# Optimization experiments

Measured on AMD Instinct MI355X. Metric: run time of the kernel, lower is better.

The kernel has to match this reference:

```python
import jax, jax.numpy as jnp
import numpy as np

D_IN, D_HID, D_OUT, N_EXP, N_TOK = 1024, 4096, 1024, 8, 4096


def setup_inputs() -> dict:
    key = jax.random.key(0)
    ks = jax.random.split(key, 7)
    x = jax.random.normal(ks[0], (N_TOK, D_IN), dtype=jnp.float32)
    s1 = 1.0 / np.sqrt(D_IN).astype(np.float32)
    s2 = 1.0 / np.sqrt(D_HID).astype(np.float32)
    W1 = jax.random.uniform(ks[1], (N_EXP, D_IN, D_HID), jnp.float32, -s1, s1)
    b1 = jax.random.uniform(ks[2], (N_EXP, D_HID), jnp.float32, -s1, s1)
    W2 = jax.random.uniform(ks[3], (N_EXP, D_HID, D_OUT), jnp.float32, -s2, s2)
    b2 = jax.random.uniform(ks[4], (N_EXP, D_OUT), jnp.float32, -s2, s2)
    Wg = jax.random.uniform(ks[5], (D_IN, N_EXP), jnp.float32, -s1, s1)
    bg = jax.random.uniform(ks[6], (N_EXP,), jnp.float32, -s1, s1)
    return {"x": x, "W1": W1, "b1": b1, "W2": W2, "b2": b2,
            "Wg": Wg, "bg": bg, "top_k": 2}


def reference(x, W1, b1, W2, b2, Wg, bg, top_k):
    # Gating: softmax over experts, then top-k and renormalizing softmax.
    gates = jax.nn.softmax(x @ Wg + bg, axis=-1)            # [N, E]
    topk_vals, topk_idx = jax.lax.top_k(gates, top_k)       # [N, k]
    topk_w = jax.nn.softmax(topk_vals, axis=-1)             # [N, k]
    # Dense all-expert MLP (vectorized replacement for per-token Python loop).
    h = jax.nn.relu(jnp.einsum('nd,edh->neh', x, W1) + b1)  # [N, E, H]
    y = jnp.einsum('neh,eho->neo', h, W2) + b2              # [N, E, O]
    # Combine: gather each token's top-k expert outputs, weighted sum.
    sel = jnp.take_along_axis(y, topk_idx[:, :, None], axis=1)  # [N, k, O]
    out = jnp.sum(topk_w[:, :, None] * sel, axis=1)             # [N, O]
    return out
```

## Files before the change

### kernel.cpp

```cpp
#include <hip/hip_runtime.h>
#include <hip/hip_bf16.h>

#define NTOK 4096
#define DIN  1024
#define DHID 4096
#define DOUT 1024
#define NEXP 8
#define TMAX 72
#define G1BLK (TMAX * (DHID / 128))
#define SPLITK 2
#define KH (DHID / SPLITK)

typedef __hip_bfloat16 bf16;
typedef short short8 __attribute__((ext_vector_type(8)));
typedef short short4v __attribute__((ext_vector_type(4)));
typedef float floatx4 __attribute__((ext_vector_type(4)));

#define WAIT_VM0 0x0F70
#define WAIT_VM4 0x0F74

#define WS_XB    0ull
#define WS_W1T   8388608ull
#define WS_W2T   75497472ull
#define WS_H     142606336ull
#define WS_META  209715200ull
#define MO_CNT    0
#define MO_CURG   32
#define MO_T2I    1536
#define MO_T2W    34304
#define MO_ROWS   67072
#define MO_ROWW   99840

__device__ __forceinline__ void gload16(const bf16* g, bf16* l) {
  __builtin_amdgcn_global_load_lds(
      (const __attribute__((address_space(1))) void*)g,
      (__attribute__((address_space(3))) void*)l, 16, 0, 0);
}

__device__ __forceinline__ int tile_lookup(const int* __restrict__ cnt, int tile,
                                           int& e, int& start, int& mrows) {
  int o = 0, tacc = 0;
  e = -1; start = 0; mrows = 0;
  #pragma unroll
  for (int k = 0; k < 8; k++) {
    int c = cnt[k];
    int nb = (c + 127) >> 7;
    if (e < 0 && tile < tacc + nb) {
      e = k; int r = (tile - tacc) << 7;
      start = o + r; mrows = min(128, c - r);
    }
    tacc += nb; o += c;
  }
  return tacc;
}

__device__ __forceinline__ void transpose_tile(const float* __restrict__ in,
                                               bf16* __restrict__ out,
                                               int R, int C, int cx, int ry,
                                               int e, float* t) {
  size_t ebase = (size_t)e * R * C;
  int c0 = cx * 64, r0 = ry * 64;
  int tid = threadIdx.x;
  int rr = tid >> 4;
  int cq = (tid & 15) * 4;
  #pragma unroll
  for (int i = 0; i < 4; i++) {
    int r = rr + i * 16;
    float4 v = *(const float4*)(in + ebase + (size_t)(r0 + r) * C + c0 + cq);
    t[(cq + 0) * 65 + r] = v.x; t[(cq + 1) * 65 + r] = v.y;
    t[(cq + 2) * 65 + r] = v.z; t[(cq + 3) * 65 + r] = v.w;
  }
  __syncthreads();
  int cc = tid >> 3;
  int rq = (tid & 7) * 8;
  #pragma unroll
  for (int i = 0; i < 2; i++) {
    int c = cc + i * 32;
    union { int4 v; bf16 h[8]; } u;
    #pragma unroll
    for (int j = 0; j < 8; j++) u.h[j] = __float2bfloat16(t[c * 65 + rq + j]);
    *(int4*)(out + ebase + (size_t)(c0 + c) * R + r0 + rq) = u.v;
  }
}

__device__ __forceinline__ void gate_body(const float* __restrict__ x,
                                          const float* __restrict__ Wg,
                                          const float* __restrict__ bg,
                                          bf16* __restrict__ xb,
                                          int* __restrict__ t2i,
                                          float* __restrict__ t2w,
                                          int* __restrict__ cnt, int blk) {
  int wave = threadIdx.x >> 6, lane = threadIdx.x & 63;
  int t = blk * 4 + wave;
  const float* xr = x + (size_t)t * DIN;
  bf16* xbr = xb + (size_t)t * DIN;
  float acc[8] = {0.f, 0.f, 0.f, 0.f, 0.f, 0.f, 0.f, 0.f};
  #pragma unroll
  for (int i = 0; i < 4; i++) {
    int d0 = (lane + i * 64) * 4;
    float4 v = *(const float4*)(xr + d0);
    union { short4v s; bf16 h[4]; } u;
    u.h[0] = __float2bfloat16(v.x); u.h[1] = __float2bfloat16(v.y);
    u.h[2] = __float2bfloat16(v.z); u.h[3] = __float2bfloat16(v.w);
    *(short4v*)(xbr + d0) = u.s;
    float xv4[4] = {v.x, v.y, v.z, v.w};
    #pragma unroll
    for (int c = 0; c < 4; c++) {
      const float* wr = Wg + (size_t)(d0 + c) * 8;
      float4 w0 = *(const float4*)wr;
      float4 w1 = *(const float4*)(wr + 4);
      float xv = xv4[c];
      acc[0] += xv * w0.x; acc[1] += xv * w0.y; acc[2] += xv * w0.z; acc[3] += xv * w0.w;
      acc[4] += xv * w1.x; acc[5] += xv * w1.y; acc[6] += xv * w1.z; acc[7] += xv * w1.w;
    }
  }
  #pragma unroll
  for (int off = 32; off; off >>= 1) {
    #pragma unroll
    for (int e = 0; e < 8; e++) acc[e] += __shfl_xor(acc[e], off, 64);
  }
  if (lane == 0) {
    float p[8], m = -1e30f, s = 0.f;
    #pragma unroll
    for (int e = 0; e < 8; e++) { p[e] = acc[e] + bg[e]; m = fmaxf(m, p[e]); }
    #pragma unroll
    for (int e = 0; e < 8; e++) { p[e] = expf(p[e] - m); s += p[e]; }
    float inv = 1.f / s;
    #pragma unroll
    for (int e = 0; e < 8; e++) p[e] *= inv;
    int i0 = 0;
    #pragma unroll
    for (int e = 1; e < 8; e++) if (p[e] > p[i0]) i0 = e;
    int i1 = (i0 == 0) ? 1 : 0;
    #pragma unroll
    for (int e = 0; e < 8; e++) if (e != i0 && p[e] > p[i1]) i1 = e;
    float d = expf(p[i1] - p[i0]);
    float w0 = 1.f / (1.f + d), w1 = d / (1.f + d);
    t2i[2 * t] = i0; t2i[2 * t + 1] = i1;
    t2w[2 * t] = w0; t2w[2 * t + 1] = w1;
    atomicAdd(&cnt[i0], 1);
    atomicAdd(&cnt[i1], 1);
  }
}

__global__ __launch_bounds__(256)
void k_gate_w1t(const float* __restrict__ x, const float* __restrict__ Wg,
                const float* __restrict__ bg, bf16* __restrict__ xb,
                int* __restrict__ t2i, float* __restrict__ t2w,
                int* __restrict__ cnt,
                const float* __restrict__ W1, bf16* __restrict__ w1t) {
  __shared__ __align__(16) float tsm[64 * 65];
  int b = blockIdx.x;
  if (b < NTOK / 4) {
    gate_body(x, Wg, bg, xb, t2i, t2w, cnt, b);
  } else {
    int tb = b - NTOK / 4;
    int e = tb >> 10;
    int rem = tb & 1023;
    int cx = rem & 63;
    int ry = rem >> 6;
    transpose_tile(W1, w1t, DIN, DHID, cx, ry, e, tsm);
  }
}

__global__ void k_scatter(const int* __restrict__ t2i, const float* __restrict__ t2w,
                          const int* __restrict__ cnt, int* __restrict__ cur_g,
                          int* __restrict__ rows, float* __restrict__ roww) {
  __shared__ int lcnt[8], lbase[8];
  if (threadIdx.x < 8) lcnt[threadIdx.x] = 0;
  __syncthreads();
  int t = blockIdx.x * 256 + threadIdx.x;
  int e0 = t2i[2 * t], e1 = t2i[2 * t + 1];
  int p0 = atomicAdd(&lcnt[e0], 1);
  int p1 = atomicAdd(&lcnt[e1], 1);
  __syncthreads();
  if (threadIdx.x < 8) {
    int base = atomicAdd(&cur_g[threadIdx.x], lcnt[threadIdx.x]);
    int off = 0;
    for (int k = 0; k < threadIdx.x; k++) off += cnt[k];
    lbase[threadIdx.x] = off + base;
  }
  __syncthreads();
  int a0 = lbase[e0] + p0, a1 = lbase[e1] + p1;
  rows[a0] = t; roww[a0] = t2w[2 * t];
  rows[a1] = t; roww[a1] = t2w[2 * t + 1];
}

template <int MODE>
__device__ __forceinline__ void gemm_tile(
    const bf16* __restrict__ A, const bf16* __restrict__ Bt,
    const float* __restrict__ bias, const int* __restrict__ cnt,
    const int* __restrict__ rows, const float* __restrict__ roww,
    bf16* __restrict__ hout, float* __restrict__ out,
    int K, int N, int hwid, int kbase, int nk, bool addb,
    bf16 (&Al)[3][4096], bf16 (&Bl)[3][4096]) {
  int xcd = hwid & 7, pos = hwid >> 3;
  int tile = xcd * 9 + pos % 9;
  int e, start, mrows;
  int ntt = tile_lookup(cnt, tile, e, start, mrows);
  if (tile >= ntt) return;
  int n0 = (pos / 9) * 128;
  int tid = threadIdx.x, lane = tid & 63, wave = tid >> 6;
  int wm = wave & 1, wn = wave >> 1;

  int srow = tid >> 2;
  int rot = (srow >> 1) & 3;
  int kc8 = (((tid & 3) - rot) & 3) * 8;
  int ra0 = srow, ra1 = 64 + srow;
  int er0 = ra0 < mrows ? ra0 : 0;
  int er1 = ra1 < mrows ? ra1 : 0;
  size_t ga0, ga1;
  if (MODE == 1) {
    ga0 = (size_t)rows[start + er0] * K;
    ga1 = (size_t)rows[start + er1] * K;
  } else {
    ga0 = (size_t)(start + er0) * K;
    ga1 = (size_t)(start + er1) * K;
  }
  const bf16* ap0 = A + ga0 + kbase + kc8;
  const bf16* ap1 = A + ga1 + kbase + kc8;
  const bf16* bb = Bt + (size_t)e * K * N + (size_t)n0 * K + kbase;
  const bf16* bp0 = bb + (size_t)srow * K + kc8;
  const bf16* bp1 = bb + (size_t)(64 + srow) * K + kc8;

  floatx4 zz = {0.f, 0.f, 0.f, 0.f};
  floatx4 acc[4][4];
  #pragma unroll
  for (int i = 0; i < 4; i++)
    #pragma unroll
    for (int j = 0; j < 4; j++) acc[i][j] = zz;

  int fr = lane & 15;
  int ko = (((lane >> 4) + ((fr >> 1) & 3)) & 3) * 8;

#define STAGE(buf, kk)                                    \
  do {                                                    \
    gload16(ap0 + (kk), &Al[buf][tid * 8]);               \
    gload16(ap1 + (kk), &Al[buf][2048 + tid * 8]);        \
    gload16(bp0 + (kk), &Bl[buf][tid * 8]);               \
    gload16(bp1 + (kk), &Bl[buf][2048 + tid * 8]);        \
  } while (0)

  STAGE(0, 0);
  STAGE(1, 32);

  int cur = 0;
  for (int t = 0; t < nk; ++t) {
    if (t + 1 < nk) __builtin_amdgcn_s_waitcnt(WAIT_VM4);
    else            __builtin_amdgcn_s_waitcnt(WAIT_VM0);
    __builtin_amdgcn_s_barrier();

    short8 af[4], bfr[4];
    #pragma unroll
    for (int i = 0; i < 4; i++)
      af[i] = *(const short8*)&Al[cur][(wm * 64 + i * 16 + fr) * 32 + ko];
    #pragma unroll
    for (int j = 0; j < 4; j++)
      bfr[j] = *(const short8*)&Bl[cur][(wn * 64 + j * 16 + fr) * 32 + ko];

    if (t + 2 < nk) {
      int nb = cur + 2; if (nb >= 3) nb -= 3;
      STAGE(nb, (t + 2) * 32);
    }

    #pragma unroll
    for (int i = 0; i < 4; i++)
      #pragma unroll
      for (int j = 0; j < 4; j++)
        acc[i][j] = __builtin_amdgcn_mfma_f32_16x16x32_bf16(af[i], bfr[j], acc[i][j], 0, 0, 0);
    cur = (cur + 1 == 3) ? 0 : cur + 1;
  }
#undef STAGE

  int col_l = lane & 15, quad = lane >> 4;
  if (MODE == 1) {
    #pragma unroll
    for (int i = 0; i < 4; i++) {
      #pragma unroll
      for (int r = 0; r < 4; r++) {
        int row = wm * 64 + i * 16 + quad * 4 + r;
        if (row < mrows) {
          size_t rb = (size_t)(start + row) * N;
          #pragma unroll
          for (int j = 0; j < 4; j++) {
            int col = n0 + wn * 64 + j * 16 + col_l;
            float v = acc[i][j][r] + bias[e * N + col];
            hout[rb + col] = __float2bfloat16(fmaxf(v, 0.f));
          }
        }
      }
    }
  } else {
    #pragma unroll
    for (int i = 0; i < 4; i++) {
      #pragma unroll
      for (int r = 0; r < 4; r++) {
        int row = wm * 64 + i * 16 + quad * 4 + r;
        if (row < mrows) {
          int tok = rows[start + row];
          float w = roww[start + row];
          size_t ob = (size_t)tok * N;
          #pragma unroll
          for (int j = 0; j < 4; j++) {
            int col = n0 + wn * 64 + j * 16 + col_l;
            float b = addb ? bias[e * N + col] : 0.f;
            float v = (acc[i][j][r] + b) * w;
            unsafeAtomicAdd(&out[ob + col], v);
          }
        }
      }
    }
  }
}

__global__ __launch_bounds__(256)
void k_gemm1_w2t(const bf16* __restrict__ A, const bf16* __restrict__ Bt,
                 const float* __restrict__ bias, const int* __restrict__ cnt,
                 const int* __restrict__ rows, const float* __restrict__ roww,
                 bf16* __restrict__ hout,
                 const float* __restrict__ W2, bf16* __restrict__ w2t) {
  __shared__ __align__(16) char smem[49152];
  int b = blockIdx.x;
  if (b < G1BLK) {
    auto& Al = *reinterpret_cast<bf16(*)[3][4096]>((void*)smem);
    auto& Bl = *reinterpret_cast<bf16(*)[3][4096]>((void*)(smem + 24576));
    gemm_tile<1>(A, Bt, bias, cnt, rows, roww, hout, nullptr,
                 DIN, DHID, b, 0, DIN / 32, true, Al, Bl);
  } else {
    int tb = b - G1BLK;
    int e = tb >> 10;
    int rem = tb & 1023;
    int cx = rem & 15;
    int ry = rem >> 4;
    transpose_tile(W2, w2t, DHID, DOUT, cx, ry, e, (float*)smem);
  }
}

__global__ __launch_bounds__(256)
void k_gemm2(const bf16* __restrict__ A, const bf16* __restrict__ Bt,
             const float* __restrict__ bias, const int* __restrict__ cnt,
             const int* __restrict__ rows, const float* __restrict__ roww,
             float* __restrict__ out) {
  __shared__ bf16 Al[3][4096];
  __shared__ bf16 Bl[3][4096];
  int hwid = blockIdx.x + blockIdx.y * gridDim.x;
  gemm_tile<2>(A, Bt, bias, cnt, rows, roww, nullptr, out,
               DHID, DOUT, hwid, blockIdx.z * KH, KH / 32, blockIdx.z == 0,
               Al, Bl);
}

extern "C" void kernel_launch(void* const* d_in, const int* in_sizes, int n_in,
                              void* d_out, int out_size, void* d_ws, size_t ws_size,
                              hipStream_t stream) {
  const float* x  = (const float*)d_in[0];
  const float* W1 = (const float*)d_in[1];
  const float* b1 = (const float*)d_in[2];
  const float* W2 = (const float*)d_in[3];
  const float* b2 = (const float*)d_in[4];
  const float* Wg = (const float*)d_in[5];
  const float* bg = (const float*)d_in[6];
  float* out = (float*)d_out;
  char* ws = (char*)d_ws;

  bf16* xb  = (bf16*)(ws + WS_XB);
  bf16* w1t = (bf16*)(ws + WS_W1T);
  bf16* w2t = (bf16*)(ws + WS_W2T);
  bf16* h   = (bf16*)(ws + WS_H);
  char* meta = ws + WS_META;
  int*   cnt    = (int*)(meta + MO_CNT);
  int*   cur_g  = (int*)(meta + MO_CURG);
  int*   t2i    = (int*)(meta + MO_T2I);
  float* t2w    = (float*)(meta + MO_T2W);
  int*   rows   = (int*)(meta + MO_ROWS);
  float* roww   = (float*)(meta + MO_ROWW);

  hipMemsetAsync(meta, 0, 64, stream);
  hipMemsetAsync(d_out, 0, (size_t)out_size * sizeof(float), stream);

  k_gate_w1t<<<NTOK / 4 + 8192, 256, 0, stream>>>(x, Wg, bg, xb, t2i, t2w, cnt,
                                                  W1, w1t);
  k_scatter<<<NTOK / 256, 256, 0, stream>>>(t2i, t2w, cnt, cur_g, rows, roww);
  k_gemm1_w2t<<<G1BLK + 8192, 256, 0, stream>>>(xb, w1t, b1, cnt, rows, roww, h,
                                                W2, w2t);
  k_gemm2<<<dim3(TMAX, DOUT / 128, SPLITK), 256, 0, stream>>>(
      h, w2t, b2, cnt, rows, roww, out);
}
```

Baseline: 638.4 us.

## Fold memsets and W2 transpose into prep kernel; single-block ballot scatter; drop split-K

The two memsets are gone: output zeroing and the W2 transpose now run as extra blocks of the prep kernel. Gating no longer does global atomics for counts. A single 1024-thread block builds expert counts and row assignments with wave ballots and prefix sums. GEMM1 now runs as a plain kernel, and GEMM2 drops split-K, halving its grid and its atomic traffic. The intent is to cut launch and memset overhead and atomic contention, at the cost of less overlap of the W2 transpose with GEMM1 and lower parallelism in GEMM2.

```diff
diff --git a/kernel.cpp b/kernel.cpp
--- a/kernel.cpp
+++ b/kernel.cpp
@@ -7,9 +7,6 @@
 #define DOUT 1024
 #define NEXP 8
 #define TMAX 72
-#define G1BLK (TMAX * (DHID / 128))
-#define SPLITK 2
-#define KH (DHID / SPLITK)
 
 typedef __hip_bfloat16 bf16;
 typedef short short8 __attribute__((ext_vector_type(8)));
@@ -25,11 +22,19 @@
 #define WS_H     142606336ull
 #define WS_META  209715200ull
 #define MO_CNT    0
-#define MO_CURG   32
 #define MO_T2I    1536
 #define MO_T2W    34304
 #define MO_ROWS   67072
 #define MO_ROWW   99840
+
+#define PREP_GATE (NTOK / 4)
+#define PREP_W1T  8192
+#define PREP_W2T  8192
+#define PREP_OUTZ 256
+#define PREP_B1   (PREP_GATE)
+#define PREP_B2   (PREP_B1 + PREP_W1T)
+#define PREP_B3   (PREP_B2 + PREP_W2T)
+#define PREP_NBLK (PREP_B3 + PREP_OUTZ)
 
 __device__ __forceinline__ void gload16(const bf16* g, bf16* l) {
   __builtin_amdgcn_global_load_lds(
@@ -88,8 +93,7 @@
                                           const float* __restrict__ bg,
                                           bf16* __restrict__ xb,
                                           int* __restrict__ t2i,
-                                          float* __restrict__ t2w,
-                                          int* __restrict__ cnt, int blk) {
+                                          float* __restrict__ t2w, int blk) {
   int wave = threadIdx.x >> 6, lane = threadIdx.x & 63;
   int t = blk * 4 + wave;
   const float* xr = x + (size_t)t * DIN;
@@ -138,52 +142,98 @@
     float w0 = 1.f / (1.f + d), w1 = d / (1.f + d);
     t2i[2 * t] = i0; t2i[2 * t + 1] = i1;
     t2w[2 * t] = w0; t2w[2 * t + 1] = w1;
-    atomicAdd(&cnt[i0], 1);
-    atomicAdd(&cnt[i1], 1);
   }
 }
 
 __global__ __launch_bounds__(256)
-void k_gate_w1t(const float* __restrict__ x, const float* __restrict__ Wg,
-                const float* __restrict__ bg, bf16* __restrict__ xb,
-                int* __restrict__ t2i, float* __restrict__ t2w,
-                int* __restrict__ cnt,
-                const float* __restrict__ W1, bf16* __restrict__ w1t) {
+void k_prep(const float* __restrict__ x, const float* __restrict__ Wg,
+            const float* __restrict__ bg, bf16* __restrict__ xb,
+            int* __restrict__ t2i, float* __restrict__ t2w,
+            const float* __restrict__ W1, bf16* __restrict__ w1t,
+            const float* __restrict__ W2, bf16* __restrict__ w2t,
+            float* __restrict__ out) {
   __shared__ __align__(16) float tsm[64 * 65];
   int b = blockIdx.x;
-  if (b < NTOK / 4) {
-    gate_body(x, Wg, bg, xb, t2i, t2w, cnt, b);
-  } else {
-    int tb = b - NTOK / 4;
+  if (b < PREP_B1) {
+    gate_body(x, Wg, bg, xb, t2i, t2w, b);
+  } else if (b < PREP_B2) {
+    int tb = b - PREP_B1;
     int e = tb >> 10;
     int rem = tb & 1023;
     int cx = rem & 63;
     int ry = rem >> 6;
     transpose_tile(W1, w1t, DIN, DHID, cx, ry, e, tsm);
-  }
-}
-
-__global__ void k_scatter(const int* __restrict__ t2i, const float* __restrict__ t2w,
-                          const int* __restrict__ cnt, int* __restrict__ cur_g,
-                          int* __restrict__ rows, float* __restrict__ roww) {
-  __shared__ int lcnt[8], lbase[8];
-  if (threadIdx.x < 8) lcnt[threadIdx.x] = 0;
+  } else if (b < PREP_B3) {
+    int tb = b - PREP_B2;
+    int e = tb >> 10;
+    int rem = tb & 1023;
+    int cx = rem & 15;
+    int ry = rem >> 4;
+    transpose_tile(W2, w2t, DHID, DOUT, cx, ry, e, tsm);
+  } else {
+    int t = (b - PREP_B3) * 256 + threadIdx.x;
+    float4 z = {0.f, 0.f, 0.f, 0.f};
+    float4* o4 = (float4*)out;
+    #pragma unroll
+    for (int i = 0; i < 16; i++) o4[i * 65536 + t] = z;
+  }
+}
+
+__global__ __launch_bounds__(1024)
+void k_scatter(const int* __restrict__ t2i, const float* __restrict__ t2w,
+               int* __restrict__ cnt, int* __restrict__ rows,
+               float* __restrict__ roww) {
+  __shared__ int wtot[16][8];
+  int tid = threadIdx.x, wave = tid >> 6, lane = tid & 63;
+  unsigned long long ltmask = (1ull << lane) - 1ull;
+  int e0c[4], e1c[4], r0c[4], r1c[4];
+  int wcnt[8] = {0, 0, 0, 0, 0, 0, 0, 0};
+  #pragma unroll
+  for (int c = 0; c < 4; c++) {
+    int t = wave * 256 + c * 64 + lane;
+    int e0 = t2i[2 * t], e1 = t2i[2 * t + 1];
+    e0c[c] = e0; e1c[c] = e1;
+    r0c[c] = 0; r1c[c] = 0;
+    #pragma unroll
+    for (int e = 0; e < 8; e++) {
+      unsigned long long m0 = __ballot(e0 == e);
+      unsigned long long m1 = __ballot(e1 == e);
+      int c0 = __popcll(m0), c1 = __popcll(m1);
+      if (e0 == e) r0c[c] = wcnt[e] + __popcll(m0 & ltmask);
+      if (e1 == e) r1c[c] = wcnt[e] + c0 + __popcll(m1 & ltmask);
+      wcnt[e] += c0 + c1;
+    }
+  }
+  if (lane < 8) wtot[wave][lane] = wcnt[lane];
   __syncthreads();
-  int t = blockIdx.x * 256 + threadIdx.x;
-  int e0 = t2i[2 * t], e1 = t2i[2 * t + 1];
-  int p0 = atomicAdd(&lcnt[e0], 1);
-  int p1 = atomicAdd(&lcnt[e1], 1);
-  __syncthreads();
-  if (threadIdx.x < 8) {
-    int base = atomicAdd(&cur_g[threadIdx.x], lcnt[threadIdx.x]);
-    int off = 0;
-    for (int k = 0; k < threadIdx.x; k++) off += cnt[k];
-    lbase[threadIdx.x] = off + base;
-  }
-  __syncthreads();
-  int a0 = lbase[e0] + p0, a1 = lbase[e1] + p1;
-  rows[a0] = t; roww[a0] = t2w[2 * t];
-  rows[a1] = t; roww[a1] = t2w[2 * t + 1];
+  int base_e[8];
+  {
+    int tote[8];
+    #pragma unroll
+    for (int e = 0; e < 8; e++) {
+      int s = 0;
+      #pragma unroll
+      for (int w = 0; w < 16; w++) s += wtot[w][e];
+      tote[e] = s;
+    }
+    int a = 0;
+    #pragma unroll
+    for (int e = 0; e < 8; e++) {
+      int p = 0;
+      for (int w = 0; w < wave; w++) p += wtot[w][e];
+      base_e[e] = a + p;
+      a += tote[e];
+    }
+    if (tid < 8) cnt[tid] = tote[tid];
+  }
+  #pragma unroll
+  for (int c = 0; c < 4; c++) {
+    int t = wave * 256 + c * 64 + lane;
+    int a0 = base_e[e0c[c]] + r0c[c];
+    int a1 = base_e[e1c[c]] + r1c[c];
+    rows[a0] = t; roww[a0] = t2w[2 * t];
+    rows[a1] = t; roww[a1] = t2w[2 * t + 1];
+  }
 }
 
 template <int MODE>
@@ -192,7 +242,7 @@
     const float* __restrict__ bias, const int* __restrict__ cnt,
     const int* __restrict__ rows, const float* __restrict__ roww,
     bf16* __restrict__ hout, float* __restrict__ out,
-    int K, int N, int hwid, int kbase, int nk, bool addb,
+    int K, int N, int hwid,
     bf16 (&Al)[3][4096], bf16 (&Bl)[3][4096]) {
   int xcd = hwid & 7, pos = hwid >> 3;
   int tile = xcd * 9 + pos % 9;
@@ -217,9 +267,9 @@
     ga0 = (size_t)(start + er0) * K;
     ga1 = (size_t)(start + er1) * K;
   }
-  const bf16* ap0 = A + ga0 + kbase + kc8;
-  const bf16* ap1 = A + ga1 + kbase + kc8;
-  const bf16* bb = Bt + (size_t)e * K * N + (size_t)n0 * K + kbase;
+  const bf16* ap0 = A + ga0 + kc8;
+  const bf16* ap1 = A + ga1 + kc8;
+  const bf16* bb = Bt + (size_t)e * K * N + (size_t)n0 * K;
   const bf16* bp0 = bb + (size_t)srow * K + kc8;
   const bf16* bp1 = bb + (size_t)(64 + srow) * K + kc8;
 
@@ -244,6 +294,7 @@
   STAGE(0, 0);
   STAGE(1, 32);
 
+  int nk = K >> 5;
   int cur = 0;
   for (int t = 0; t < nk; ++t) {
     if (t + 1 < nk) __builtin_amdgcn_s_waitcnt(WAIT_VM4);
@@ -303,8 +354,7 @@
           #pragma unroll
           for (int j = 0; j < 4; j++) {
             int col = n0 + wn * 64 + j * 16 + col_l;
-            float b = addb ? bias[e * N + col] : 0.f;
-            float v = (acc[i][j][r] + b) * w;
+            float v = (acc[i][j][r] + bias[e * N + col]) * w;
             unsafeAtomicAdd(&out[ob + col], v);
           }
         }
@@ -314,26 +364,15 @@
 }
 
 __global__ __launch_bounds__(256)
-void k_gemm1_w2t(const bf16* __restrict__ A, const bf16* __restrict__ Bt,
-                 const float* __restrict__ bias, const int* __restrict__ cnt,
-                 const int* __restrict__ rows, const float* __restrict__ roww,
-                 bf16* __restrict__ hout,
-                 const float* __restrict__ W2, bf16* __restrict__ w2t) {
-  __shared__ __align__(16) char smem[49152];
-  int b = blockIdx.x;
-  if (b < G1BLK) {
-    auto& Al = *reinterpret_cast<bf16(*)[3][4096]>((void*)smem);
-    auto& Bl = *reinterpret_cast<bf16(*)[3][4096]>((void*)(smem + 24576));
-    gemm_tile<1>(A, Bt, bias, cnt, rows, roww, hout, nullptr,
-                 DIN, DHID, b, 0, DIN / 32, true, Al, Bl);
-  } else {
-    int tb = b - G1BLK;
-    int e = tb >> 10;
-    int rem = tb & 1023;
-    int cx = rem & 15;
-    int ry = rem >> 4;
-    transpose_tile(W2, w2t, DHID, DOUT, cx, ry, e, (float*)smem);
-  }
+void k_gemm1(const bf16* __restrict__ A, const bf16* __restrict__ Bt,
+             const float* __restrict__ bias, const int* __restrict__ cnt,
+             const int* __restrict__ rows, const float* __restrict__ roww,
+             bf16* __restrict__ hout) {
+  __shared__ bf16 Al[3][4096];
+  __shared__ bf16 Bl[3][4096];
+  int hwid = blockIdx.x + blockIdx.y * gridDim.x;
+  gemm_tile<1>(A, Bt, bias, cnt, rows, roww, hout, nullptr,
+               DIN, DHID, hwid, Al, Bl);
 }
 
 __global__ __launch_bounds__(256)
@@ -345,8 +384,7 @@
   __shared__ bf16 Bl[3][4096];
   int hwid = blockIdx.x + blockIdx.y * gridDim.x;
   gemm_tile<2>(A, Bt, bias, cnt, rows, roww, nullptr, out,
-               DHID, DOUT, hwid, blockIdx.z * KH, KH / 32, blockIdx.z == 0,
-               Al, Bl);
+               DHID, DOUT, hwid, Al, Bl);
 }
 
 extern "C" void kernel_launch(void* const* d_in, const int* in_sizes, int n_in,
@@ -367,21 +405,17 @@
   bf16* w2t = (bf16*)(ws + WS_W2T);
   bf16* h   = (bf16*)(ws + WS_H);
   char* meta = ws + WS_META;
-  int*   cnt    = (int*)(meta + MO_CNT);
-  int*   cur_g  = (int*)(meta + MO_CURG);
-  int*   t2i    = (int*)(meta + MO_T2I);
-  float* t2w    = (float*)(meta + MO_T2W);
-  int*   rows   = (int*)(meta + MO_ROWS);
-  float* roww   = (float*)(meta + MO_ROWW);
-
-  hipMemsetAsync(meta, 0, 64, stream);
-  hipMemsetAsync(d_out, 0, (size_t)out_size * sizeof(float), stream);
-
-  k_gate_w1t<<<NTOK / 4 + 8192, 256, 0, stream>>>(x, Wg, bg, xb, t2i, t2w, cnt,
-                                                  W1, w1t);
-  k_scatter<<<NTOK / 256, 256, 0, stream>>>(t2i, t2w, cnt, cur_g, rows, roww);
-  k_gemm1_w2t<<<G1BLK + 8192, 256, 0, stream>>>(xb, w1t, b1, cnt, rows, roww, h,
-                                                W2, w2t);
-  k_gemm2<<<dim3(TMAX, DOUT / 128, SPLITK), 256, 0, stream>>>(
+  int*   cnt  = (int*)(meta + MO_CNT);
+  int*   t2i  = (int*)(meta + MO_T2I);
+  float* t2w  = (float*)(meta + MO_T2W);
+  int*   rows = (int*)(meta + MO_ROWS);
+  float* roww = (float*)(meta + MO_ROWW);
+
+  k_prep<<<PREP_NBLK, 256, 0, stream>>>(x, Wg, bg, xb, t2i, t2w,
+                                        W1, w1t, W2, w2t, out);
+  k_scatter<<<1, 1024, 0, stream>>>(t2i, t2w, cnt, rows, roww);
+  k_gemm1<<<dim3(TMAX, DHID / 128), 256, 0, stream>>>(
+      xb, w1t, b1, cnt, rows, roww, h);
+  k_gemm2<<<dim3(TMAX, DOUT / 128), 256, 0, stream>>>(
       h, w2t, b2, cnt, rows, roww, out);
 }
```

Result: faster. 582.7 us (-8.7%).
